# Kernel tuning notes

Measured on AMD Instinct MI355X. Metric: run time of the kernel, lower is better.

## Reference

```python
import jax, jax.numpy as jnp
import numpy as np

L, N, D = 4, 50000, 64        # lookback, n_nodes, gnn_dim
E = 500000                    # n_edges
HID = 256
LN_EPS = 1e-5


def setup_inputs() -> dict:
    key = jax.random.key(0)
    ks = jax.random.split(key, 8)
    h_all = jax.random.normal(ks[0], (L, N, D), dtype=jnp.float32)
    src = jax.random.randint(ks[1], (E,), 0, N, dtype=jnp.int32)
    dst = jax.random.randint(ks[2], (E,), 0, N, dtype=jnp.int32)
    W1 = jax.random.normal(ks[3], (HID, L * 2 * D), dtype=jnp.float32) * (1.0 / np.sqrt(L * 2 * D))
    b1 = jax.random.normal(ks[4], (HID,), dtype=jnp.float32) * 0.01
    W3 = jax.random.normal(ks[5], (1, HID), dtype=jnp.float32) * (1.0 / np.sqrt(HID))
    b3 = jax.random.normal(ks[6], (1,), dtype=jnp.float32) * 0.01
    gamma2 = jnp.ones((HID,), dtype=jnp.float32)
    beta2 = jnp.zeros((HID,), dtype=jnp.float32)
    return {"h_all": h_all, "src": src, "dst": dst, "W1": W1, "b1": b1,
            "W3": W3, "b3": b3, "gamma2": gamma2, "beta2": beta2}


def reference(h_all, src, dst, W1, b1, W3, b3, gamma2, beta2):
    lb, _, d = h_all.shape
    # importance weights 1..L normalized
    imp = jnp.arange(1, lb + 1, dtype=h_all.dtype)
    imp = imp / imp.sum()
    # per-edge gather of src/dst features for every lookback step: [L, E, 2D]
    hs = h_all[:, src]                                  # [L, E, D]
    hd = h_all[:, dst]                                  # [L, E, D]
    embed = jnp.concatenate([hs, hd], axis=-1) * imp[:, None, None]
    # concat over lookback steps -> [E, L*2D]
    embed = jnp.transpose(embed, (1, 0, 2)).reshape(embed.shape[1], -1)
    # MLP: W1(tanh) -> LayerNorm -> dropout(eval=identity) -> relu -> W3
    x = jnp.tanh(embed) @ W1.T + b1                     # [E, HID]
    mu = jnp.mean(x, axis=-1, keepdims=True)
    var = jnp.var(x, axis=-1, keepdims=True)
    x = (x - mu) * jax.lax.rsqrt(var + LN_EPS) * gamma2 + beta2
    x = jax.nn.relu(x)
    out = x @ W3.T + b3                                 # [E, 1]
    return out[:, 0]
```

## Files before the change

kernel.cpp:

```cpp
#include <hip/hip_runtime.h>
#include <hip/hip_bf16.h>

#define LL 4
#define NN 50000
#define DD 64
#define EE 500000
#define HID 256
#define KDIM 512
#define LN_EPS 1e-5f

typedef __bf16 bf16x8 __attribute__((ext_vector_type(8)));
typedef float f32x16 __attribute__((ext_vector_type(16)));

__device__ __forceinline__ void async16(const void* g, void* l) {
    __builtin_amdgcn_global_load_lds(
        (const __attribute__((address_space(1))) void*)g,
        (__attribute__((address_space(3))) void*)l, 16, 0, 0);
}

__global__ void tanh_conv(const float* __restrict__ h, __bf16* __restrict__ t) {
    int i = (blockIdx.x * 256 + threadIdx.x) * 8;
    int l = i / (NN * DD);
    float imp = (float)(l + 1) * 0.1f;
    const float4* p = (const float4*)(h + i);
    float4 a = p[0];
    float4 b = p[1];
    float x[8] = {a.x, a.y, a.z, a.w, b.x, b.y, b.z, b.w};
    bf16x8 r;
    #pragma unroll
    for (int j = 0; j < 8; ++j) {
        float e2 = __expf(2.0f * (imp * x[j]));
        r[j] = (__bf16)(1.0f - 2.0f / (e2 + 1.0f));
    }
    *(bf16x8*)(t + i) = r;
}

__global__ void w2_conv(const float* __restrict__ w1, __bf16* __restrict__ o) {
    int t = blockIdx.x * 256 + threadIdx.x;
    int j  = t & 511;
    int b  = t >> 9;
    int k0 = (b >> 1) * 16 + (b & 1) * 8;
    int r  = j & 255;
    int col = (k0 >> 6) * 128 + ((j >> 8) ? 64 : 0) + (k0 & 63);
    const float4* p = (const float4*)(w1 + r * KDIM + col);
    float4 va = p[0];
    float4 vb = p[1];
    bf16x8 v;
    v[0] = (__bf16)va.x; v[1] = (__bf16)va.y; v[2] = (__bf16)va.z; v[3] = (__bf16)va.w;
    v[4] = (__bf16)vb.x; v[5] = (__bf16)vb.y; v[6] = (__bf16)vb.z; v[7] = (__bf16)vb.w;
    *(bf16x8*)(o + (size_t)t * 8) = v;
}

__global__ __launch_bounds__(256, 2)
void node_proj(const __bf16* __restrict__ tb, const __bf16* __restrict__ w2c,
               __bf16* __restrict__ P) {
    __shared__ __align__(16) char smem[65536];
    __bf16* Bs = (__bf16*)smem;
    float*  Cs = (float*)smem;

    const int tid  = threadIdx.x;
    const int wave = tid >> 6;
    const int lane = tid & 63;
    const int h32  = lane >> 5;
    const int c32  = lane & 31;
    const int cb   = blockIdx.y;
    const int n00  = blockIdx.x * 128;

    #pragma unroll
    for (int it = 0; it < 16; ++it) {
        int o = it * 2048 + tid * 8;
        async16(w2c + (size_t)(o >> 10) * 4096 + cb * 1024 + (o & 1023), Bs + o);
    }

    int node = n00 + wave * 32 + c32;
    if (node >= NN) node = NN - 1;
    uint4 a[16];
    #pragma unroll
    for (int u = 0; u < 16; ++u) {
        const __bf16* p = tb + (size_t)(u >> 2) * (NN * DD) + node * DD
                        + (u & 3) * 16 + h32 * 8;
        a[u] = *(const uint4*)p;
    }

    f32x16 acc[4];
    #pragma unroll
    for (int nt = 0; nt < 4; ++nt) acc[nt] = (f32x16)(0.f);

    __syncthreads();

    #pragma unroll
    for (int u = 0; u < 16; ++u) {
        bf16x8 af = __builtin_bit_cast(bf16x8, a[u]);
        const __bf16* Bk = Bs + (u * 2 + h32) * 1024 + c32 * 8;
        #pragma unroll
        for (int nt = 0; nt < 4; ++nt) {
            bf16x8 bf = *(const bf16x8*)(Bk + nt * 256);
            acc[nt] = __builtin_amdgcn_mfma_f32_32x32x16_bf16(af, bf, acc[nt], 0, 0, 0);
        }
    }
    __syncthreads();

    #pragma unroll
    for (int nt = 0; nt < 4; ++nt) {
        #pragma unroll
        for (int r = 0; r < 16; ++r) {
            int nl = wave * 32 + (r & 3) + 8 * (r >> 2) + 4 * h32;
            Cs[nl * 128 + nt * 32 + c32] = acc[nt][r];
        }
    }
    __syncthreads();
    #pragma unroll
    for (int it = 0; it < 8; ++it) {
        int o  = it * 2048 + tid * 8;
        int nl = o >> 7;
        int n  = n00 + nl;
        if (n < NN) {
            bf16x8 v;
            #pragma unroll
            for (int z = 0; z < 8; ++z) v[z] = (__bf16)Cs[o + z];
            *(bf16x8*)(P + (size_t)n * 512 + cb * 128 + (o & 127)) = v;
        }
    }
}

__global__ __launch_bounds__(256, 3)
void edge_out(const __bf16* __restrict__ P, const int* __restrict__ src,
              const int* __restrict__ dst, const float* __restrict__ b1,
              const float* __restrict__ w3, const float* __restrict__ b3,
              const float* __restrict__ gamma, const float* __restrict__ beta,
              float* __restrict__ out) {
    const int tid = threadIdx.x;
    const int g   = tid >> 4;
    const int j   = tid & 15;

    float b1v[16], gv[16], btv[16], wv[16];
    {
        const float4* pb = (const float4*)(b1 + j * 16);
        const float4* pg = (const float4*)(gamma + j * 16);
        const float4* pt = (const float4*)(beta + j * 16);
        const float4* pw = (const float4*)(w3 + j * 16);
        #pragma unroll
        for (int z = 0; z < 4; ++z) {
            float4 vb = pb[z], vg = pg[z], vt = pt[z], vw = pw[z];
            b1v[z*4+0] = vb.x; b1v[z*4+1] = vb.y; b1v[z*4+2] = vb.z; b1v[z*4+3] = vb.w;
            gv [z*4+0] = vg.x; gv [z*4+1] = vg.y; gv [z*4+2] = vg.z; gv [z*4+3] = vg.w;
            btv[z*4+0] = vt.x; btv[z*4+1] = vt.y; btv[z*4+2] = vt.z; btv[z*4+3] = vt.w;
            wv [z*4+0] = vw.x; wv [z*4+1] = vw.y; wv [z*4+2] = vw.z; wv [z*4+3] = vw.w;
        }
    }
    const float b3v = b3[0];
    const int e0 = blockIdx.x * 128 + g * 8;

    uint4 cs0, cs1, cd0, cd1, ns0, ns1, nd0, nd1;
    {
        int ec = e0 < EE ? e0 : EE - 1;
        int s = src[ec], d = dst[ec];
        const uint4* ps = (const uint4*)(P + (size_t)s * 512 + j * 16);
        const uint4* pd = (const uint4*)(P + (size_t)d * 512 + 256 + j * 16);
        cs0 = ps[0]; cs1 = ps[1]; cd0 = pd[0]; cd1 = pd[1];
    }
    #pragma unroll
    for (int i = 0; i < 8; ++i) {
        if (i < 7) {
            int e = e0 + i + 1;
            int ec = e < EE ? e : EE - 1;
            int s = src[ec], d = dst[ec];
            const uint4* ps = (const uint4*)(P + (size_t)s * 512 + j * 16);
            const uint4* pd = (const uint4*)(P + (size_t)d * 512 + 256 + j * 16);
            ns0 = ps[0]; ns1 = ps[1]; nd0 = pd[0]; nd1 = pd[1];
        }
        bf16x8 a0 = __builtin_bit_cast(bf16x8, cs0);
        bf16x8 a1 = __builtin_bit_cast(bf16x8, cs1);
        bf16x8 c0 = __builtin_bit_cast(bf16x8, cd0);
        bf16x8 c1 = __builtin_bit_cast(bf16x8, cd1);
        float x[16];
        #pragma unroll
        for (int z = 0; z < 8; ++z) {
            x[z]     = (float)a0[z] + (float)c0[z] + b1v[z];
            x[z + 8] = (float)a1[z] + (float)c1[z] + b1v[z + 8];
        }
        float sum = 0.f, sq = 0.f;
        #pragma unroll
        for (int z = 0; z < 16; ++z) {
            sum += x[z];
            sq   = fmaf(x[z], x[z], sq);
        }
        #pragma unroll
        for (int m = 1; m < 16; m <<= 1) {
            sum += __shfl_xor(sum, m);
            sq  += __shfl_xor(sq,  m);
        }
        float mu = sum * (1.0f / 256.0f);
        float rs = rsqrtf(sq * (1.0f / 256.0f) - mu * mu + LN_EPS);
        float dot = 0.f;
        #pragma unroll
        for (int z = 0; z < 16; ++z) {
            float y = fmaxf((x[z] - mu) * rs * gv[z] + btv[z], 0.f);
            dot = fmaf(y, wv[z], dot);
        }
        #pragma unroll
        for (int m = 1; m < 16; m <<= 1) dot += __shfl_xor(dot, m);
        int e = e0 + i;
        if (j == 0 && e < EE) out[e] = dot + b3v;
        cs0 = ns0; cs1 = ns1; cd0 = nd0; cd1 = nd1;
    }
}

extern "C" void kernel_launch(void* const* d_in, const int* in_sizes, int n_in,
                              void* d_out, int out_size, void* d_ws, size_t ws_size,
                              hipStream_t stream) {
    const float* h_all  = (const float*)d_in[0];
    const int*   src    = (const int*)  d_in[1];
    const int*   dst    = (const int*)  d_in[2];
    const float* W1     = (const float*)d_in[3];
    const float* b1     = (const float*)d_in[4];
    const float* W3     = (const float*)d_in[5];
    const float* b3     = (const float*)d_in[6];
    const float* gamma2 = (const float*)d_in[7];
    const float* beta2  = (const float*)d_in[8];
    float* out = (float*)d_out;

    __bf16* tb  = (__bf16*)d_ws;
    __bf16* w2c = tb + (size_t)LL * NN * DD;
    __bf16* P   = w2c + 131072;

    tanh_conv<<<6250, 256, 0, stream>>>(h_all, tb);
    w2_conv<<<64, 256, 0, stream>>>(W1, w2c);
    node_proj<<<dim3((NN + 127) / 128, 4), 256, 0, stream>>>(tb, w2c, P);
    edge_out<<<(EE + 127) / 128, 256, 0, stream>>>(P, src, dst, b1, W3, b3,
                                                   gamma2, beta2, out);
}
```

Before: 204.9 us.

## Fold b1 into node projection and deepen edge gather prefetch with shuffled indices

Moves the b1 bias add into node_proj's dst-half output, so edge_out no longer holds b1 registers or performs the add. edge_out now loads src/dst indices once per 16-lane group and broadcasts them with shuffles instead of reloading them each iteration. The feature prefetch grows from one edge ahead to two, using a three-slot register ring, so more gather latency is hidden. The cost is more VGPRs, which may reduce occupancy, and the bias is now rounded into bf16 P.

```diff
diff --git a/kernel.cpp b/kernel.cpp
--- a/kernel.cpp
+++ b/kernel.cpp
@@ -53,7 +53,7 @@
 
 __global__ __launch_bounds__(256, 2)
 void node_proj(const __bf16* __restrict__ tb, const __bf16* __restrict__ w2c,
-               __bf16* __restrict__ P) {
+               const float* __restrict__ b1, __bf16* __restrict__ P) {
     __shared__ __align__(16) char smem[65536];
     __bf16* Bs = (__bf16*)smem;
     float*  Cs = (float*)smem;
@@ -72,6 +72,20 @@
         async16(w2c + (size_t)(o >> 10) * 4096 + cb * 1024 + (o & 1023), Bs + o);
     }
 
+    float badd[8];
+    {
+        int c0 = (tid * 8) & 127;
+        if (cb >= 2) {
+            const float4* pb = (const float4*)(b1 + (cb - 2) * 128 + c0);
+            float4 u = pb[0], v = pb[1];
+            badd[0] = u.x; badd[1] = u.y; badd[2] = u.z; badd[3] = u.w;
+            badd[4] = v.x; badd[5] = v.y; badd[6] = v.z; badd[7] = v.w;
+        } else {
+            #pragma unroll
+            for (int z = 0; z < 8; ++z) badd[z] = 0.f;
+        }
+    }
+
     int node = n00 + wave * 32 + c32;
     if (node >= NN) node = NN - 1;
     uint4 a[16];
@@ -117,7 +131,7 @@
         if (n < NN) {
             bf16x8 v;
             #pragma unroll
-            for (int z = 0; z < 8; ++z) v[z] = (__bf16)Cs[o + z];
+            for (int z = 0; z < 8; ++z) v[z] = (__bf16)(Cs[o + z] + badd[z]);
             *(bf16x8*)(P + (size_t)n * 512 + cb * 128 + (o & 127)) = v;
         }
     }
@@ -125,7 +139,7 @@
 
 __global__ __launch_bounds__(256, 3)
 void edge_out(const __bf16* __restrict__ P, const int* __restrict__ src,
-              const int* __restrict__ dst, const float* __restrict__ b1,
+              const int* __restrict__ dst,
               const float* __restrict__ w3, const float* __restrict__ b3,
               const float* __restrict__ gamma, const float* __restrict__ beta,
               float* __restrict__ out) {
@@ -133,16 +147,14 @@
     const int g   = tid >> 4;
     const int j   = tid & 15;
 
-    float b1v[16], gv[16], btv[16], wv[16];
+    float gv[16], btv[16], wv[16];
     {
-        const float4* pb = (const float4*)(b1 + j * 16);
         const float4* pg = (const float4*)(gamma + j * 16);
         const float4* pt = (const float4*)(beta + j * 16);
         const float4* pw = (const float4*)(w3 + j * 16);
         #pragma unroll
         for (int z = 0; z < 4; ++z) {
-            float4 vb = pb[z], vg = pg[z], vt = pt[z], vw = pw[z];
-            b1v[z*4+0] = vb.x; b1v[z*4+1] = vb.y; b1v[z*4+2] = vb.z; b1v[z*4+3] = vb.w;
+            float4 vg = pg[z], vt = pt[z], vw = pw[z];
             gv [z*4+0] = vg.x; gv [z*4+1] = vg.y; gv [z*4+2] = vg.z; gv [z*4+3] = vg.w;
             btv[z*4+0] = vt.x; btv[z*4+1] = vt.y; btv[z*4+2] = vt.z; btv[z*4+3] = vt.w;
             wv [z*4+0] = vw.x; wv [z*4+1] = vw.y; wv [z*4+2] = vw.z; wv [z*4+3] = vw.w;
@@ -151,33 +163,42 @@
     const float b3v = b3[0];
     const int e0 = blockIdx.x * 128 + g * 8;
 
-    uint4 cs0, cs1, cd0, cd1, ns0, ns1, nd0, nd1;
-    {
-        int ec = e0 < EE ? e0 : EE - 1;
-        int s = src[ec], d = dst[ec];
+    int ep = e0 + (j & 7);
+    if (ep >= EE) ep = EE - 1;
+    const int sj = src[ep];
+    const int dj = dst[ep];
+
+    uint4 s0[3], s1[3], d0[3], d1[3];
+
+    #pragma unroll
+    for (int i = 0; i < 2; ++i) {
+        int s = __shfl(sj, i, 16);
+        int d = __shfl(dj, i, 16);
         const uint4* ps = (const uint4*)(P + (size_t)s * 512 + j * 16);
         const uint4* pd = (const uint4*)(P + (size_t)d * 512 + 256 + j * 16);
-        cs0 = ps[0]; cs1 = ps[1]; cd0 = pd[0]; cd1 = pd[1];
-    }
+        s0[i] = ps[0]; s1[i] = ps[1]; d0[i] = pd[0]; d1[i] = pd[1];
+    }
+
     #pragma unroll
     for (int i = 0; i < 8; ++i) {
-        if (i < 7) {
-            int e = e0 + i + 1;
-            int ec = e < EE ? e : EE - 1;
-            int s = src[ec], d = dst[ec];
+        if (i + 2 < 8) {
+            const int slot = (i + 2) % 3;
+            int s = __shfl(sj, i + 2, 16);
+            int d = __shfl(dj, i + 2, 16);
             const uint4* ps = (const uint4*)(P + (size_t)s * 512 + j * 16);
             const uint4* pd = (const uint4*)(P + (size_t)d * 512 + 256 + j * 16);
-            ns0 = ps[0]; ns1 = ps[1]; nd0 = pd[0]; nd1 = pd[1];
-        }
-        bf16x8 a0 = __builtin_bit_cast(bf16x8, cs0);
-        bf16x8 a1 = __builtin_bit_cast(bf16x8, cs1);
-        bf16x8 c0 = __builtin_bit_cast(bf16x8, cd0);
-        bf16x8 c1 = __builtin_bit_cast(bf16x8, cd1);
+            s0[slot] = ps[0]; s1[slot] = ps[1]; d0[slot] = pd[0]; d1[slot] = pd[1];
+        }
+        const int cs = i % 3;
+        bf16x8 a0 = __builtin_bit_cast(bf16x8, s0[cs]);
+        bf16x8 a1 = __builtin_bit_cast(bf16x8, s1[cs]);
+        bf16x8 c0 = __builtin_bit_cast(bf16x8, d0[cs]);
+        bf16x8 c1 = __builtin_bit_cast(bf16x8, d1[cs]);
         float x[16];
         #pragma unroll
         for (int z = 0; z < 8; ++z) {
-            x[z]     = (float)a0[z] + (float)c0[z] + b1v[z];
-            x[z + 8] = (float)a1[z] + (float)c1[z] + b1v[z + 8];
+            x[z]     = (float)a0[z] + (float)c0[z];
+            x[z + 8] = (float)a1[z] + (float)c1[z];
         }
         float sum = 0.f, sq = 0.f;
         #pragma unroll
@@ -202,8 +223,11 @@
         for (int m = 1; m < 16; m <<= 1) dot += __shfl_xor(dot, m);
         int e = e0 + i;
         if (j == 0 && e < EE) out[e] = dot + b3v;
-        cs0 = ns0; cs1 = ns1; cd0 = nd0; cd1 = nd1;
-    }
+    }
+
+    #pragma unroll
+    for (int z = 0; z < 16; ++z)
+        asm volatile("" :: "v"(gv[z]), "v"(btv[z]), "v"(wv[z]));
 }
 
 extern "C" void kernel_launch(void* const* d_in, const int* in_sizes, int n_in,
@@ -226,7 +250,7 @@
 
     tanh_conv<<<6250, 256, 0, stream>>>(h_all, tb);
     w2_conv<<<64, 256, 0, stream>>>(W1, w2c);
-    node_proj<<<dim3((NN + 127) / 128, 4), 256, 0, stream>>>(tb, w2c, P);
-    edge_out<<<(EE + 127) / 128, 256, 0, stream>>>(P, src, dst, b1, W3, b3,
+    node_proj<<<dim3((NN + 127) / 128, 4), 256, 0, stream>>>(tb, w2c, b1, P);
+    edge_out<<<(EE + 127) / 128, 256, 0, stream>>>(P, src, dst, W3, b3,
                                                    gamma2, beta2, out);
 }
```

Result: no change. 201.7 us (-1.6%).
